# Optimization experiments

Measured on AMD Instinct MI355X. Metric: run time of the kernel, lower is better.

The kernel has to match this reference:

```python
import jax, jax.numpy as jnp
import numpy as np
from jax import lax

FIR_TAPS = np.array([1.0, 3.0, 3.0, 1.0], dtype=np.float32)
FACTOR = 2
GAIN = 1.0


def _fir_kernel(C):
    # _setup_kernel: outer product, normalize to sum 1; upsample scales by gain*factor**2
    k = np.outer(FIR_TAPS, FIR_TAPS)
    k = k / k.sum() * (GAIN * FACTOR ** 2)  # 4x4 kernel, sum == 4
    k = jnp.asarray(k, jnp.float32)
    return jnp.tile(k[None, None], (C, 1, 1, 1))  # [C,1,4,4] depthwise


def setup_inputs() -> dict:
    key = jax.random.key(0)
    k1, k2, k3 = jax.random.split(key, 3)
    x = jax.random.normal(k1, (16, 256, 64, 64), jnp.float32)
    W = jax.random.normal(k2, (256, 256, 3, 3), jnp.float32) * 0.02
    b = jax.random.normal(k3, (256,), jnp.float32) * 0.02
    return {"x": x, "W": W, "b": b}


def reference(x, W, b):
    B, C, H, Wd = x.shape
    kern = _fir_kernel(C)
    # upfirdn2d upsample: zero-insert by 2 (lhs_dilation), pad0=2 / pad1=1(+up-1=2),
    # depthwise FIR correlation -> [B, C, 2H, 2W]
    p0, p1 = 2, 2  # pad1 = p//2 + (factor-1) trailing zeros folded into padding
    h = lax.conv_general_dilated(
        x, kern, window_strides=(1, 1), padding=((p0, p1), (p0, p1)),
        lhs_dilation=(FACTOR, FACTOR),
        dimension_numbers=("NCHW", "OIHW", "NCHW"), feature_group_count=C)
    # 3x3 conv, padding=1, stride=1 -> [B, out_ch, 2H, 2W]
    y = lax.conv_general_dilated(
        h, W, window_strides=(1, 1), padding=((1, 1), (1, 1)),
        dimension_numbers=("NCHW", "OIHW", "NCHW"))
    return y + b[None, :, None, None]
```

## Files before the change

kernel.cpp:

```cpp
#include <hip/hip_runtime.h>
#include <hip/hip_bf16.h>
#include <stdint.h>

typedef __attribute__((ext_vector_type(8))) short bf16x8;
typedef __attribute__((ext_vector_type(4))) float f32x4;

#define PH 130
#define NT 36

__device__ __forceinline__ short f2bf(float f) {
  uint32_t u = __builtin_bit_cast(uint32_t, f);
  u = (u + 0x7FFFu + ((u >> 16) & 1u)) >> 16;
  return (short)u;
}

__device__ __forceinline__ void gload16(const void* g, void* l) {
  __builtin_amdgcn_global_load_lds(
      (const __attribute__((address_space(1))) void*)g,
      (__attribute__((address_space(3))) void*)l, 16, 0, 0);
}

__global__ void wpack(const float* __restrict__ W, short* __restrict__ A) {
  int tid = blockIdx.x * 256 + threadIdx.x;
  if (tid >= 256 * 2304) return;
  int co = tid / 2304;
  int r  = tid - co * 2304;
  int tap = r >> 8, ci = r & 255;
  A[tid] = f2bf(W[((size_t)(co * 256 + ci)) * 9 + tap]);
}

__global__ void fir_up(const float* __restrict__ x, short* __restrict__ hT) {
  const int bp = blockIdx.x;
  const int b = bp / PH, pp = bp - b * PH;
  const int ci0 = blockIdx.y << 6;
  const int t = threadIdx.x;
  short* outrow = hT + ((size_t)(b * PH + pp) * PH) * 256 + ci0;

  if (pp == 0 || pp == PH - 1) {
    for (int idx = t; idx < PH * 64; idx += 256) {
      int qp = idx >> 6, c = idx & 63;
      outrow[(size_t)qp * 256 + c] = 0;
    }
    return;
  }
  const int p = pp - 1;
  int i0, i1; float wr0, wr1;
  if (!(p & 1)) { i0 = (p >> 1) - 1; i1 = p >> 1;     wr0 = 0.25f; wr1 = 0.75f; }
  else          { i0 = p >> 1;       i1 = (p >> 1)+1; wr0 = 0.75f; wr1 = 0.25f; }

  __shared__ float X[2][64][65];
#pragma unroll
  for (int r = 0; r < 2; ++r) {
    int ir = r ? i1 : i0;
    bool ok = (ir >= 0 && ir < 64);
#pragma unroll
    for (int it = 0; it < 4; ++it) {
      int idx = it * 256 + t;
      int ci = idx >> 4, jq = idx & 15;
      f32x4 v = {0.f, 0.f, 0.f, 0.f};
      if (ok)
        v = *(const f32x4*)&x[((size_t)(b * 256 + ci0 + ci) * 64 + ir) * 64 + jq * 4];
      X[r][jq * 4 + 0][ci] = v[0];
      X[r][jq * 4 + 1][ci] = v[1];
      X[r][jq * 4 + 2][ci] = v[2];
      X[r][jq * 4 + 3][ci] = v[3];
    }
  }
  __syncthreads();

  const int c = t & 63;
  for (int qp = (t >> 6); qp < PH; qp += 4) {
    float val = 0.f;
    if (qp >= 1 && qp <= 128) {
      int q = qp - 1;
      int j0, j1; float wc0, wc1;
      if (!(q & 1)) { j0 = (q >> 1) - 1; j1 = q >> 1; wc0 = 0.25f; wc1 = 0.75f; }
      else          { j0 = q >> 1;       j1 = j0 + 1; wc0 = 0.75f; wc1 = 0.25f; }
      float v00 = (j0 >= 0) ? X[0][j0][c] : 0.f;
      float v10 = (j0 >= 0) ? X[1][j0][c] : 0.f;
      float v01 = (j1 < 64) ? X[0][j1][c] : 0.f;
      float v11 = (j1 < 64) ? X[1][j1][c] : 0.f;
      val = wr0 * (wc0 * v00 + wc1 * v01) + wr1 * (wc0 * v10 + wc1 * v11);
    }
    outrow[(size_t)qp * 256 + c] = f2bf(val);
  }
}

__global__ __launch_bounds__(512) void conv3x3_gemm(
    const short* __restrict__ hT, const short* __restrict__ Wp,
    const float* __restrict__ bias, float* __restrict__ y) {
  __shared__ short ldsA[2][16384];
  __shared__ short ldsB[2][16384];
  const int tid = threadIdx.x;
  const int lane = tid & 63, w = tid >> 6;
  const int wm = w >> 2, wn = w & 3;

  const int bid = blockIdx.x;
  const int tile = (bid & 7) * 128 + (bid >> 3);
  const int b = tile >> 6, p0 = (tile & 63) * 2;

  const short* srcA[4];
  const short* srcB[4];
#pragma unroll
  for (int h = 0; h < 2; ++h)
#pragma unroll
    for (int i = 0; i < 2; ++i) {
      int o = h * 16384 + i * 8192 + w * 1024 + lane * 16;
      int L = o ^ (((o >> 7) & 7) << 4);
      int row = L >> 7, kk = (L & 127) >> 1;
      int pr = row >> 7, q = row & 127;
      srcA[h * 2 + i] = hT + ((size_t)((b * PH + p0 + pr) * PH + q)) * 256 + kk;
      srcB[h * 2 + i] = Wp + (size_t)row * 2304 + kk;
    }

  auto offA = [&](int t) {
    int tap = t >> 2, ci0 = (t & 3) << 6;
    int dm = tap / 3, dn = tap - dm * 3;
    return (dm * PH + dn) * 256 + ci0;
  };
  auto offB = [&](int t) { return (t >> 2) * 256 + ((t & 3) << 6); };

  auto stageA = [&](int t, int h) {
    int o = offA(t);
    short* dst = &ldsA[t & 1][h * 8192];
#pragma unroll
    for (int i = 0; i < 2; ++i)
      gload16(srcA[h * 2 + i] + o, dst + i * 4096 + w * 512);
  };
  auto stageB = [&](int t, int h) {
    int o = offB(t);
    short* dst = &ldsB[t & 1][h * 8192];
#pragma unroll
    for (int i = 0; i < 2; ++i)
      gload16(srcB[h * 2 + i] + o, dst + i * 4096 + w * 512);
  };

  int aP[2], bP[2];
#pragma unroll
  for (int ks = 0; ks < 2; ++ks) {
    int La = (wm * 128 + (lane & 15)) * 128 + (lane >> 4) * 16 + ks * 64;
    aP[ks] = La ^ ((lane & 7) << 4);
    int Lb = (wn * 64 + (lane & 15)) * 128 + (lane >> 4) * 16 + ks * 64;
    bP[ks] = Lb ^ ((lane & 7) << 4);
  }

  f32x4 acc[8][4];
#pragma unroll
  for (int m = 0; m < 8; ++m)
#pragma unroll
    for (int n = 0; n < 4; ++n) acc[m][n] = (f32x4){0.f, 0.f, 0.f, 0.f};

  stageB(0, 0); stageB(0, 1); stageA(0, 0); stageA(0, 1);
  stageB(1, 0); stageB(1, 1); stageA(1, 0);
  asm volatile("s_waitcnt vmcnt(6)" ::: "memory");
  __builtin_amdgcn_s_barrier();

  for (int t = 0; t < NT; ++t) {
    const char* LA = (const char*)&ldsA[t & 1][0];
    const char* LB = (const char*)&ldsB[t & 1][0];

    bf16x8 a0[4], a1[4], b0[4], b1[4];
#pragma unroll
    for (int m = 0; m < 4; ++m) {
      a0[m] = *(const bf16x8*)(LA + aP[0] + m * 2048);
      a1[m] = *(const bf16x8*)(LA + aP[1] + m * 2048);
    }
#pragma unroll
    for (int n = 0; n < 4; ++n)
      b0[n] = *(const bf16x8*)(LB + bP[0] + n * 2048);
    if (t + 1 < NT) stageA(t + 1, 1);
    __builtin_amdgcn_s_barrier();
    asm volatile("s_waitcnt lgkmcnt(0)" ::: "memory");
    __builtin_amdgcn_sched_barrier(0);
    __builtin_amdgcn_s_setprio(1);
#pragma unroll
    for (int m = 0; m < 4; ++m)
#pragma unroll
      for (int n = 0; n < 4; ++n)
        acc[m][n] = __builtin_amdgcn_mfma_f32_16x16x32_bf16(a0[m], b0[n], acc[m][n], 0, 0, 0);
    __builtin_amdgcn_s_setprio(0);
    __builtin_amdgcn_s_barrier();

#pragma unroll
    for (int n = 0; n < 4; ++n)
      b1[n] = *(const bf16x8*)(LB + bP[1] + n * 2048);
    __builtin_amdgcn_s_barrier();
    asm volatile("s_waitcnt lgkmcnt(0)" ::: "memory");
    __builtin_amdgcn_sched_barrier(0);
    __builtin_amdgcn_s_setprio(1);
#pragma unroll
    for (int m = 0; m < 4; ++m)
#pragma unroll
      for (int n = 0; n < 4; ++n)
        acc[m][n] = __builtin_amdgcn_mfma_f32_16x16x32_bf16(a1[m], b1[n], acc[m][n], 0, 0, 0);
    __builtin_amdgcn_s_setprio(0);
    __builtin_amdgcn_s_barrier();

    bf16x8 c0[4], c1[4];
#pragma unroll
    for (int m = 0; m < 4; ++m) {
      c0[m] = *(const bf16x8*)(LA + aP[0] + (m + 4) * 2048);
      c1[m] = *(const bf16x8*)(LA + aP[1] + (m + 4) * 2048);
    }
    if (t + 2 < NT) stageB(t + 2, 0);
    __builtin_amdgcn_s_barrier();
    asm volatile("s_waitcnt lgkmcnt(0)" ::: "memory");
    __builtin_amdgcn_sched_barrier(0);
    __builtin_amdgcn_s_setprio(1);
#pragma unroll
    for (int m = 0; m < 4; ++m)
#pragma unroll
      for (int n = 0; n < 4; ++n)
        acc[m + 4][n] = __builtin_amdgcn_mfma_f32_16x16x32_bf16(c0[m], b0[n], acc[m + 4][n], 0, 0, 0);
    __builtin_amdgcn_s_setprio(0);
    __builtin_amdgcn_s_barrier();

    if (t + 2 < NT) { stageB(t + 2, 1); stageA(t + 2, 0); }
    __builtin_amdgcn_sched_barrier(0);
    __builtin_amdgcn_s_setprio(1);
#pragma unroll
    for (int m = 0; m < 4; ++m)
#pragma unroll
      for (int n = 0; n < 4; ++n)
        acc[m + 4][n] = __builtin_amdgcn_mfma_f32_16x16x32_bf16(c1[m], b1[n], acc[m + 4][n], 0, 0, 0);
    __builtin_amdgcn_s_setprio(0);
    if (t == NT - 2)      asm volatile("s_waitcnt vmcnt(0)" ::: "memory");
    else if (t < NT - 2)  asm volatile("s_waitcnt vmcnt(6)" ::: "memory");
    __builtin_amdgcn_s_barrier();
  }

#pragma unroll
  for (int n = 0; n < 4; ++n) {
    int co = wn * 64 + n * 16 + (lane & 15);
    float bv = bias[co];
    float* yp = y + (((size_t)(b * 256 + co)) * 128 + (p0 + wm)) * 128;
#pragma unroll
    for (int m = 0; m < 8; ++m) {
      int q0 = m * 16 + ((lane >> 4) << 2);
      f32x4 v = acc[m][n];
      v[0] += bv; v[1] += bv; v[2] += bv; v[3] += bv;
      *(f32x4*)(yp + q0) = v;
    }
  }
}

extern "C" void kernel_launch(void* const* d_in, const int* in_sizes, int n_in,
                              void* d_out, int out_size, void* d_ws, size_t ws_size,
                              hipStream_t stream) {
  const float* x    = (const float*)d_in[0];
  const float* W    = (const float*)d_in[1];
  const float* bias = (const float*)d_in[2];
  float* y = (float*)d_out;

  const size_t hT_bytes = (size_t)16 * PH * PH * 256 * 2;
  const size_t A_bytes  = (size_t)256 * 2304 * 2;
  if (ws_size < hT_bytes + A_bytes) return;

  short* hT = (short*)d_ws;
  short* Wp = (short*)((char*)d_ws + hT_bytes);

  wpack<<<(256 * 2304 + 255) / 256, 256, 0, stream>>>(W, Wp);
  dim3 g1(16 * PH, 4);
  fir_up<<<g1, 256, 0, stream>>>(x, hT);
  conv3x3_gemm<<<1024, 512, 0, stream>>>(hT, Wp, bias, y);
}
```

Baseline: 438.0 us.

## Merge GEMM K-sub-phases into two barrier phases with whole-tile prefetch

Restructures the conv3x3 GEMM main loop from four MFMA phases separated by barriers into two. Both K halves of B are now read up front, and each accumulator gets its two K-slices in one phase. Global-to-LDS staging moves from split half-tile loads to whole-tile stageA(t+1)/stageB(t+2) calls, with the vmcnt waits adjusted to match, and the trailing barrier on the last iteration is dropped. The aim is to cut barrier and synchronisation overhead, but issuing two dependent MFMAs back to back on the same accumulator can stall on MFMA latency, and keeping more fragments live raises register pressure.

```diff
diff --git a/kernel.cpp b/kernel.cpp
--- a/kernel.cpp
+++ b/kernel.cpp
@@ -115,24 +115,25 @@
 
   auto offA = [&](int t) {
     int tap = t >> 2, ci0 = (t & 3) << 6;
-    int dm = tap / 3, dn = tap - dm * 3;
+    int dm = (tap >= 6) ? 2 : (tap >= 3) ? 1 : 0;
+    int dn = tap - 3 * dm;
     return (dm * PH + dn) * 256 + ci0;
   };
   auto offB = [&](int t) { return (t >> 2) * 256 + ((t & 3) << 6); };
 
-  auto stageA = [&](int t, int h) {
+  auto stageA = [&](int t) {
     int o = offA(t);
-    short* dst = &ldsA[t & 1][h * 8192];
-#pragma unroll
-    for (int i = 0; i < 2; ++i)
-      gload16(srcA[h * 2 + i] + o, dst + i * 4096 + w * 512);
+    short* dst = &ldsA[t & 1][0];
+#pragma unroll
+    for (int j = 0; j < 4; ++j)
+      gload16(srcA[j] + o, dst + (j >> 1) * 8192 + (j & 1) * 4096 + w * 512);
   };
-  auto stageB = [&](int t, int h) {
+  auto stageB = [&](int t) {
     int o = offB(t);
-    short* dst = &ldsB[t & 1][h * 8192];
-#pragma unroll
-    for (int i = 0; i < 2; ++i)
-      gload16(srcB[h * 2 + i] + o, dst + i * 4096 + w * 512);
+    short* dst = &ldsB[t & 1][0];
+#pragma unroll
+    for (int j = 0; j < 4; ++j)
+      gload16(srcB[j] + o, dst + (j >> 1) * 8192 + (j & 1) * 4096 + w * 512);
   };
 
   int aP[2], bP[2];
@@ -150,9 +151,8 @@
 #pragma unroll
     for (int n = 0; n < 4; ++n) acc[m][n] = (f32x4){0.f, 0.f, 0.f, 0.f};
 
-  stageB(0, 0); stageB(0, 1); stageA(0, 0); stageA(0, 1);
-  stageB(1, 0); stageB(1, 1); stageA(1, 0);
-  asm volatile("s_waitcnt vmcnt(6)" ::: "memory");
+  stageB(0); stageA(0); stageB(1);
+  asm volatile("s_waitcnt vmcnt(4)" ::: "memory");
   __builtin_amdgcn_s_barrier();
 
   for (int t = 0; t < NT; ++t) {
@@ -166,9 +166,11 @@
       a1[m] = *(const bf16x8*)(LA + aP[1] + m * 2048);
     }
 #pragma unroll
-    for (int n = 0; n < 4; ++n)
+    for (int n = 0; n < 4; ++n) {
       b0[n] = *(const bf16x8*)(LB + bP[0] + n * 2048);
-    if (t + 1 < NT) stageA(t + 1, 1);
+      b1[n] = *(const bf16x8*)(LB + bP[1] + n * 2048);
+    }
+    if (t + 1 < NT) stageA(t + 1);
     __builtin_amdgcn_s_barrier();
     asm volatile("s_waitcnt lgkmcnt(0)" ::: "memory");
     __builtin_amdgcn_sched_barrier(0);
@@ -176,14 +178,20 @@
 #pragma unroll
     for (int m = 0; m < 4; ++m)
 #pragma unroll
-      for (int n = 0; n < 4; ++n)
+      for (int n = 0; n < 4; ++n) {
         acc[m][n] = __builtin_amdgcn_mfma_f32_16x16x32_bf16(a0[m], b0[n], acc[m][n], 0, 0, 0);
+        acc[m][n] = __builtin_amdgcn_mfma_f32_16x16x32_bf16(a1[m], b1[n], acc[m][n], 0, 0, 0);
+      }
     __builtin_amdgcn_s_setprio(0);
     __builtin_amdgcn_s_barrier();
 
-#pragma unroll
-    for (int n = 0; n < 4; ++n)
-      b1[n] = *(const bf16x8*)(LB + bP[1] + n * 2048);
+    bf16x8 c0[4], c1[4];
+#pragma unroll
+    for (int m = 0; m < 4; ++m) {
+      c0[m] = *(const bf16x8*)(LA + aP[0] + (m + 4) * 2048);
+      c1[m] = *(const bf16x8*)(LA + aP[1] + (m + 4) * 2048);
+    }
+    if (t + 2 < NT) stageB(t + 2);
     __builtin_amdgcn_s_barrier();
     asm volatile("s_waitcnt lgkmcnt(0)" ::: "memory");
     __builtin_amdgcn_sched_barrier(0);
@@ -191,42 +199,14 @@
 #pragma unroll
     for (int m = 0; m < 4; ++m)
 #pragma unroll
-      for (int n = 0; n < 4; ++n)
-        acc[m][n] = __builtin_amdgcn_mfma_f32_16x16x32_bf16(a1[m], b1[n], acc[m][n], 0, 0, 0);
-    __builtin_amdgcn_s_setprio(0);
-    __builtin_amdgcn_s_barrier();
-
-    bf16x8 c0[4], c1[4];
-#pragma unroll
-    for (int m = 0; m < 4; ++m) {
-      c0[m] = *(const bf16x8*)(LA + aP[0] + (m + 4) * 2048);
-      c1[m] = *(const bf16x8*)(LA + aP[1] + (m + 4) * 2048);
-    }
-    if (t + 2 < NT) stageB(t + 2, 0);
-    __builtin_amdgcn_s_barrier();
-    asm volatile("s_waitcnt lgkmcnt(0)" ::: "memory");
-    __builtin_amdgcn_sched_barrier(0);
-    __builtin_amdgcn_s_setprio(1);
-#pragma unroll
-    for (int m = 0; m < 4; ++m)
-#pragma unroll
-      for (int n = 0; n < 4; ++n)
+      for (int n = 0; n < 4; ++n) {
         acc[m + 4][n] = __builtin_amdgcn_mfma_f32_16x16x32_bf16(c0[m], b0[n], acc[m + 4][n], 0, 0, 0);
-    __builtin_amdgcn_s_setprio(0);
-    __builtin_amdgcn_s_barrier();
-
-    if (t + 2 < NT) { stageB(t + 2, 1); stageA(t + 2, 0); }
-    __builtin_amdgcn_sched_barrier(0);
-    __builtin_amdgcn_s_setprio(1);
-#pragma unroll
-    for (int m = 0; m < 4; ++m)
-#pragma unroll
-      for (int n = 0; n < 4; ++n)
         acc[m + 4][n] = __builtin_amdgcn_mfma_f32_16x16x32_bf16(c1[m], b1[n], acc[m + 4][n], 0, 0, 0);
+      }
     __builtin_amdgcn_s_setprio(0);
     if (t == NT - 2)      asm volatile("s_waitcnt vmcnt(0)" ::: "memory");
-    else if (t < NT - 2)  asm volatile("s_waitcnt vmcnt(6)" ::: "memory");
-    __builtin_amdgcn_s_barrier();
+    else if (t < NT - 2)  asm volatile("s_waitcnt vmcnt(4)" ::: "memory");
+    if (t < NT - 1) __builtin_amdgcn_s_barrier();
   }
 
 #pragma unroll
```

Measured after the change: 429.5 us. No clear change (-1.9%).

## Make conv GEMM persistent over four tiles with two-stage unrolled K loop

Applied to the files above, without the earlier changes.

The conv3x3 GEMM now launches 256 workgroups, and each one loops over four output tiles, roughly one per CU, instead of launching 1024 single-tile workgroups. The K loop is unrolled by two so the LDS double-buffer indices become compile-time constants. The MFMA phases are regrouped into N-halves with interleaved k-steps, and lgkmcnt waits are relaxed. This aims to cut launch and tail overhead and the cost of buffer addressing. In exchange, the pipeline drains and refills at every tile boundary, and there is less parallelism to hide latency.

```diff
diff --git a/kernel.cpp b/kernel.cpp
--- a/kernel.cpp
+++ b/kernel.cpp
@@ -7,6 +7,7 @@
 
 #define PH 130
 #define NT 36
+#define ITERS 18
 
 __device__ __forceinline__ short f2bf(float f) {
   uint32_t u = __builtin_bit_cast(uint32_t, f);
@@ -96,10 +97,9 @@
   const int wm = w >> 2, wn = w & 3;
 
   const int bid = blockIdx.x;
-  const int tile = (bid & 7) * 128 + (bid >> 3);
-  const int b = tile >> 6, p0 = (tile & 63) * 2;
-
-  const short* srcA[4];
+  const int jblk = (bid & 7) * 32 + (bid >> 3);
+
+  int aRow[4], aKk[4];
   const short* srcB[4];
 #pragma unroll
   for (int h = 0; h < 2; ++h)
@@ -108,32 +108,9 @@
       int o = h * 16384 + i * 8192 + w * 1024 + lane * 16;
       int L = o ^ (((o >> 7) & 7) << 4);
       int row = L >> 7, kk = (L & 127) >> 1;
-      int pr = row >> 7, q = row & 127;
-      srcA[h * 2 + i] = hT + ((size_t)((b * PH + p0 + pr) * PH + q)) * 256 + kk;
+      aRow[h * 2 + i] = row; aKk[h * 2 + i] = kk;
       srcB[h * 2 + i] = Wp + (size_t)row * 2304 + kk;
     }
-
-  auto offA = [&](int t) {
-    int tap = t >> 2, ci0 = (t & 3) << 6;
-    int dm = tap / 3, dn = tap - dm * 3;
-    return (dm * PH + dn) * 256 + ci0;
-  };
-  auto offB = [&](int t) { return (t >> 2) * 256 + ((t & 3) << 6); };
-
-  auto stageA = [&](int t, int h) {
-    int o = offA(t);
-    short* dst = &ldsA[t & 1][h * 8192];
-#pragma unroll
-    for (int i = 0; i < 2; ++i)
-      gload16(srcA[h * 2 + i] + o, dst + i * 4096 + w * 512);
-  };
-  auto stageB = [&](int t, int h) {
-    int o = offB(t);
-    short* dst = &ldsB[t & 1][h * 8192];
-#pragma unroll
-    for (int i = 0; i < 2; ++i)
-      gload16(srcB[h * 2 + i] + o, dst + i * 4096 + w * 512);
-  };
 
   int aP[2], bP[2];
 #pragma unroll
@@ -144,102 +121,215 @@
     bP[ks] = Lb ^ ((lane & 7) << 4);
   }
 
-  f32x4 acc[8][4];
-#pragma unroll
-  for (int m = 0; m < 8; ++m)
-#pragma unroll
-    for (int n = 0; n < 4; ++n) acc[m][n] = (f32x4){0.f, 0.f, 0.f, 0.f};
-
-  stageB(0, 0); stageB(0, 1); stageA(0, 0); stageA(0, 1);
-  stageB(1, 0); stageB(1, 1); stageA(1, 0);
-  asm volatile("s_waitcnt vmcnt(6)" ::: "memory");
-  __builtin_amdgcn_s_barrier();
-
-  for (int t = 0; t < NT; ++t) {
-    const char* LA = (const char*)&ldsA[t & 1][0];
-    const char* LB = (const char*)&ldsB[t & 1][0];
-
-    bf16x8 a0[4], a1[4], b0[4], b1[4];
-#pragma unroll
-    for (int m = 0; m < 4; ++m) {
-      a0[m] = *(const bf16x8*)(LA + aP[0] + m * 2048);
-      a1[m] = *(const bf16x8*)(LA + aP[1] + m * 2048);
-    }
-#pragma unroll
-    for (int n = 0; n < 4; ++n)
-      b0[n] = *(const bf16x8*)(LB + bP[0] + n * 2048);
-    if (t + 1 < NT) stageA(t + 1, 1);
+  const char* LA0 = (const char*)&ldsA[0][0];
+  const char* LB0 = (const char*)&ldsB[0][0];
+  const char* LA1 = (const char*)&ldsA[1][0];
+  const char* LB1 = (const char*)&ldsB[1][0];
+
+  for (int mi = 0; mi < 4; ++mi) {
+    const int tau = jblk * 4 + mi;
+    const int b = tau >> 6, p0 = (tau & 63) * 2;
+
+    const short* srcA[4];
+#pragma unroll
+    for (int j = 0; j < 4; ++j)
+      srcA[j] = hT + ((size_t)((b * PH + p0 + (aRow[j] >> 7)) * PH + (aRow[j] & 127))) * 256 + aKk[j];
+
+    auto offA = [&](int t) {
+      int tap = t >> 2, ci0 = (t & 3) << 6;
+      int dm = (tap >= 6) ? 2 : (tap >= 3) ? 1 : 0;
+      int dn = tap - 3 * dm;
+      return (dm * PH + dn) * 256 + ci0;
+    };
+    auto offB = [&](int t) { return (t >> 2) * 256 + ((t & 3) << 6); };
+
+    auto stageA = [&](int t, int h) {
+      int o = offA(t);
+      short* dst = &ldsA[t & 1][h * 8192];
+#pragma unroll
+      for (int i = 0; i < 2; ++i)
+        gload16(srcA[h * 2 + i] + o, dst + i * 4096 + w * 512);
+    };
+    auto stageB = [&](int t, int h) {
+      int o = offB(t);
+      short* dst = &ldsB[t & 1][h * 8192];
+#pragma unroll
+      for (int i = 0; i < 2; ++i)
+        gload16(srcB[h * 2 + i] + o, dst + i * 4096 + w * 512);
+    };
+
+    stageA(0, 0); stageB(0, 0); stageB(0, 1); stageA(0, 1);
+    stageA(1, 0); stageB(1, 0); stageB(1, 1);
+    asm volatile("s_waitcnt vmcnt(6)" ::: "memory");
     __builtin_amdgcn_s_barrier();
-    asm volatile("s_waitcnt lgkmcnt(0)" ::: "memory");
-    __builtin_amdgcn_sched_barrier(0);
-    __builtin_amdgcn_s_setprio(1);
-#pragma unroll
-    for (int m = 0; m < 4; ++m)
-#pragma unroll
-      for (int n = 0; n < 4; ++n)
-        acc[m][n] = __builtin_amdgcn_mfma_f32_16x16x32_bf16(a0[m], b0[n], acc[m][n], 0, 0, 0);
-    __builtin_amdgcn_s_setprio(0);
-    __builtin_amdgcn_s_barrier();
-
-#pragma unroll
-    for (int n = 0; n < 4; ++n)
-      b1[n] = *(const bf16x8*)(LB + bP[1] + n * 2048);
-    __builtin_amdgcn_s_barrier();
-    asm volatile("s_waitcnt lgkmcnt(0)" ::: "memory");
-    __builtin_amdgcn_sched_barrier(0);
-    __builtin_amdgcn_s_setprio(1);
-#pragma unroll
-    for (int m = 0; m < 4; ++m)
-#pragma unroll
-      for (int n = 0; n < 4; ++n)
-        acc[m][n] = __builtin_amdgcn_mfma_f32_16x16x32_bf16(a1[m], b1[n], acc[m][n], 0, 0, 0);
-    __builtin_amdgcn_s_setprio(0);
-    __builtin_amdgcn_s_barrier();
-
-    bf16x8 c0[4], c1[4];
-#pragma unroll
-    for (int m = 0; m < 4; ++m) {
-      c0[m] = *(const bf16x8*)(LA + aP[0] + (m + 4) * 2048);
-      c1[m] = *(const bf16x8*)(LA + aP[1] + (m + 4) * 2048);
-    }
-    if (t + 2 < NT) stageB(t + 2, 0);
-    __builtin_amdgcn_s_barrier();
-    asm volatile("s_waitcnt lgkmcnt(0)" ::: "memory");
-    __builtin_amdgcn_sched_barrier(0);
-    __builtin_amdgcn_s_setprio(1);
-#pragma unroll
-    for (int m = 0; m < 4; ++m)
-#pragma unroll
-      for (int n = 0; n < 4; ++n)
-        acc[m + 4][n] = __builtin_amdgcn_mfma_f32_16x16x32_bf16(c0[m], b0[n], acc[m + 4][n], 0, 0, 0);
-    __builtin_amdgcn_s_setprio(0);
-    __builtin_amdgcn_s_barrier();
-
-    if (t + 2 < NT) { stageB(t + 2, 1); stageA(t + 2, 0); }
-    __builtin_amdgcn_sched_barrier(0);
-    __builtin_amdgcn_s_setprio(1);
-#pragma unroll
-    for (int m = 0; m < 4; ++m)
-#pragma unroll
-      for (int n = 0; n < 4; ++n)
-        acc[m + 4][n] = __builtin_amdgcn_mfma_f32_16x16x32_bf16(c1[m], b1[n], acc[m + 4][n], 0, 0, 0);
-    __builtin_amdgcn_s_setprio(0);
-    if (t == NT - 2)      asm volatile("s_waitcnt vmcnt(0)" ::: "memory");
-    else if (t < NT - 2)  asm volatile("s_waitcnt vmcnt(6)" ::: "memory");
-    __builtin_amdgcn_s_barrier();
-  }
-
-#pragma unroll
-  for (int n = 0; n < 4; ++n) {
-    int co = wn * 64 + n * 16 + (lane & 15);
-    float bv = bias[co];
-    float* yp = y + (((size_t)(b * 256 + co)) * 128 + (p0 + wm)) * 128;
-#pragma unroll
-    for (int m = 0; m < 8; ++m) {
-      int q0 = m * 16 + ((lane >> 4) << 2);
-      f32x4 v = acc[m][n];
-      v[0] += bv; v[1] += bv; v[2] += bv; v[3] += bv;
-      *(f32x4*)(yp + q0) = v;
+
+    f32x4 acc[8][4];
+#pragma unroll
+    for (int m = 0; m < 8; ++m)
+#pragma unroll
+      for (int n = 0; n < 4; ++n) acc[m][n] = (f32x4){0.f, 0.f, 0.f, 0.f};
+
+    for (int i = 0; i < ITERS; ++i) {
+      const int u = 2 * i, v = u + 1;
+      const bool more = (u + 2 < NT);
+      bf16x8 a_[2][4], c_[2][4], b_[2][2], b2[2][2];
+
+#pragma unroll
+      for (int ks = 0; ks < 2; ++ks) {
+#pragma unroll
+        for (int m = 0; m < 4; ++m) a_[ks][m] = *(const bf16x8*)(LA0 + aP[ks] + m * 2048);
+#pragma unroll
+        for (int n = 0; n < 2; ++n) b_[ks][n] = *(const bf16x8*)(LB0 + bP[ks] + n * 2048);
+      }
+      stageA(v, 1);
+      asm volatile("s_waitcnt lgkmcnt(8)" ::: "memory");
+      __builtin_amdgcn_s_barrier();
+      asm volatile("s_waitcnt lgkmcnt(0)" ::: "memory");
+      __builtin_amdgcn_s_setprio(1);
+#pragma unroll
+      for (int m = 0; m < 4; ++m)
+#pragma unroll
+        for (int n = 0; n < 2; ++n) {
+          acc[m][n] = __builtin_amdgcn_mfma_f32_16x16x32_bf16(a_[0][m], b_[0][n], acc[m][n], 0, 0, 0);
+          acc[m][n] = __builtin_amdgcn_mfma_f32_16x16x32_bf16(a_[1][m], b_[1][n], acc[m][n], 0, 0, 0);
+        }
+      __builtin_amdgcn_s_setprio(0);
+      __builtin_amdgcn_s_barrier();
+
+#pragma unroll
+      for (int ks = 0; ks < 2; ++ks)
+#pragma unroll
+        for (int n = 0; n < 2; ++n) b2[ks][n] = *(const bf16x8*)(LB0 + bP[ks] + (n + 2) * 2048);
+      __builtin_amdgcn_s_barrier();
+      asm volatile("s_waitcnt lgkmcnt(0)" ::: "memory");
+      __builtin_amdgcn_s_setprio(1);
+#pragma unroll
+      for (int m = 0; m < 4; ++m)
+#pragma unroll
+        for (int n = 0; n < 2; ++n) {
+          acc[m][n + 2] = __builtin_amdgcn_mfma_f32_16x16x32_bf16(a_[0][m], b2[0][n], acc[m][n + 2], 0, 0, 0);
+          acc[m][n + 2] = __builtin_amdgcn_mfma_f32_16x16x32_bf16(a_[1][m], b2[1][n], acc[m][n + 2], 0, 0, 0);
+        }
+      __builtin_amdgcn_s_setprio(0);
+      __builtin_amdgcn_s_barrier();
+
+#pragma unroll
+      for (int ks = 0; ks < 2; ++ks)
+#pragma unroll
+        for (int m = 0; m < 4; ++m) c_[ks][m] = *(const bf16x8*)(LA0 + aP[ks] + (m + 4) * 2048);
+      if (more) stageB(u + 2, 0);
+      __builtin_amdgcn_s_barrier();
+      asm volatile("s_waitcnt lgkmcnt(0)" ::: "memory");
+      __builtin_amdgcn_s_setprio(1);
+#pragma unroll
+      for (int m = 0; m < 4; ++m)
+#pragma unroll
+        for (int n = 0; n < 2; ++n) {
+          acc[m + 4][n] = __builtin_amdgcn_mfma_f32_16x16x32_bf16(c_[0][m], b_[0][n], acc[m + 4][n], 0, 0, 0);
+          acc[m + 4][n] = __builtin_amdgcn_mfma_f32_16x16x32_bf16(c_[1][m], b_[1][n], acc[m + 4][n], 0, 0, 0);
+        }
+      __builtin_amdgcn_s_setprio(0);
+      __builtin_amdgcn_s_barrier();
+
+      if (more) { stageB(u + 2, 1); stageA(u + 2, 0); }
+      __builtin_amdgcn_s_barrier();
+      __builtin_amdgcn_s_setprio(1);
+#pragma unroll
+      for (int m = 0; m < 4; ++m)
+#pragma unroll
+        for (int n = 0; n < 2; ++n) {
+          acc[m + 4][n + 2] = __builtin_amdgcn_mfma_f32_16x16x32_bf16(c_[0][m], b2[0][n], acc[m + 4][n + 2], 0, 0, 0);
+          acc[m + 4][n + 2] = __builtin_amdgcn_mfma_f32_16x16x32_bf16(c_[1][m], b2[1][n], acc[m + 4][n + 2], 0, 0, 0);
+        }
+      __builtin_amdgcn_s_setprio(0);
+      if (more) asm volatile("s_waitcnt vmcnt(6)" ::: "memory");
+      else      asm volatile("s_waitcnt vmcnt(0)" ::: "memory");
+      __builtin_amdgcn_s_barrier();
+
+#pragma unroll
+      for (int ks = 0; ks < 2; ++ks) {
+#pragma unroll
+        for (int m = 0; m < 4; ++m) a_[ks][m] = *(const bf16x8*)(LA1 + aP[ks] + m * 2048);
+#pragma unroll
+        for (int n = 0; n < 2; ++n) b_[ks][n] = *(const bf16x8*)(LB1 + bP[ks] + n * 2048);
+      }
+      if (more) stageA(u + 2, 1);
+      asm volatile("s_waitcnt lgkmcnt(8)" ::: "memory");
+      __builtin_amdgcn_s_barrier();
+      asm volatile("s_waitcnt lgkmcnt(0)" ::: "memory");
+      __builtin_amdgcn_s_setprio(1);
+#pragma unroll
+      for (int m = 0; m < 4; ++m)
+#pragma unroll
+        for (int n = 0; n < 2; ++n) {
+          acc[m][n] = __builtin_amdgcn_mfma_f32_16x16x32_bf16(a_[0][m], b_[0][n], acc[m][n], 0, 0, 0);
+          acc[m][n] = __builtin_amdgcn_mfma_f32_16x16x32_bf16(a_[1][m], b_[1][n], acc[m][n], 0, 0, 0);
+        }
+      __builtin_amdgcn_s_setprio(0);
+      __builtin_amdgcn_s_barrier();
+
+#pragma unroll
+      for (int ks = 0; ks < 2; ++ks)
+#pragma unroll
+        for (int n = 0; n < 2; ++n) b2[ks][n] = *(const bf16x8*)(LB1 + bP[ks] + (n + 2) * 2048);
+      __builtin_amdgcn_s_barrier();
+      asm volatile("s_waitcnt lgkmcnt(0)" ::: "memory");
+      __builtin_amdgcn_s_setprio(1);
+#pragma unroll
+      for (int m = 0; m < 4; ++m)
+#pragma unroll
+        for (int n = 0; n < 2; ++n) {
+          acc[m][n + 2] = __builtin_amdgcn_mfma_f32_16x16x32_bf16(a_[0][m], b2[0][n], acc[m][n + 2], 0, 0, 0);
+          acc[m][n + 2] = __builtin_amdgcn_mfma_f32_16x16x32_bf16(a_[1][m], b2[1][n], acc[m][n + 2], 0, 0, 0);
+        }
+      __builtin_amdgcn_s_setprio(0);
+      __builtin_amdgcn_s_barrier();
+
+#pragma unroll
+      for (int ks = 0; ks < 2; ++ks)
+#pragma unroll
+        for (int m = 0; m < 4; ++m) c_[ks][m] = *(const bf16x8*)(LA1 + aP[ks] + (m + 4) * 2048);
+      if (more) stageB(u + 3, 0);
+      __builtin_amdgcn_s_barrier();
+      asm volatile("s_waitcnt lgkmcnt(0)" ::: "memory");
+      __builtin_amdgcn_s_setprio(1);
+#pragma unroll
+      for (int m = 0; m < 4; ++m)
+#pragma unroll
+        for (int n = 0; n < 2; ++n) {
+          acc[m + 4][n] = __builtin_amdgcn_mfma_f32_16x16x32_bf16(c_[0][m], b_[0][n], acc[m + 4][n], 0, 0, 0);
+          acc[m + 4][n] = __builtin_amdgcn_mfma_f32_16x16x32_bf16(c_[1][m], b_[1][n], acc[m + 4][n], 0, 0, 0);
+        }
+      __builtin_amdgcn_s_setprio(0);
+      __builtin_amdgcn_s_barrier();
+
+      if (more) { stageB(u + 3, 1); stageA(u + 3, 0); }
+      __builtin_amdgcn_s_barrier();
+      __builtin_amdgcn_s_setprio(1);
+#pragma unroll
+      for (int m = 0; m < 4; ++m)
+#pragma unroll
+        for (int n = 0; n < 2; ++n) {
+          acc[m + 4][n + 2] = __builtin_amdgcn_mfma_f32_16x16x32_bf16(c_[0][m], b2[0][n], acc[m + 4][n + 2], 0, 0, 0);
+          acc[m + 4][n + 2] = __builtin_amdgcn_mfma_f32_16x16x32_bf16(c_[1][m], b2[1][n], acc[m + 4][n + 2], 0, 0, 0);
+        }
+      __builtin_amdgcn_s_setprio(0);
+      if (more) asm volatile("s_waitcnt vmcnt(6)" ::: "memory");
+      __builtin_amdgcn_s_barrier();
+    }
+
+#pragma unroll
+    for (int n = 0; n < 4; ++n) {
+      int co = wn * 64 + n * 16 + (lane & 15);
+      float bv = bias[co];
+      float* yp = y + (((size_t)(b * 256 + co)) * 128 + (p0 + wm)) * 128;
+#pragma unroll
+      for (int m = 0; m < 8; ++m) {
+        int q0 = m * 16 + ((lane >> 4) << 2);
+        f32x4 vv = acc[m][n];
+        vv[0] += bv; vv[1] += bv; vv[2] += bv; vv[3] += bv;
+        *(f32x4*)(yp + q0) = vv;
+      }
     }
   }
 }
@@ -262,5 +352,5 @@
   wpack<<<(256 * 2304 + 255) / 256, 256, 0, stream>>>(W, Wp);
   dim3 g1(16 * PH, 4);
   fir_up<<<g1, 256, 0, stream>>>(x, hT);
-  conv3x3_gemm<<<1024, 512, 0, stream>>>(hT, Wp, bias, y);
-}
+  conv3x3_gemm<<<256, 512, 0, stream>>>(hT, Wp, bias, y);
+}
```

Result: no change. 431.2 us (-1.6%).
